# Kernel optimization log

Measured on AMD Instinct MI355X. Metric: run time of the kernel, lower is better.

## Reference

```python
import jax, jax.numpy as jnp
import numpy as np

B, SQ, SKV, E, H = 4, 2048, 2048, 1024, 16
HD = E // H  # 64


def stablemax(x):
    # StableMax: s(x) = x+1 if x>=0 else 1/(1-x), normalized along last axis
    s = jnp.where(x >= 0, x + 1.0, 1.0 / (1.0 - x))
    return s / jnp.sum(s, axis=-1, keepdims=True)


def setup_inputs() -> dict:
    key = jax.random.key(0)
    ks = jax.random.split(key, 6)
    scale = 1.0 / np.sqrt(E)
    return {
        "query": jax.random.normal(ks[0], (B, SQ, E), jnp.float32),
        "key_value": jax.random.normal(ks[1], (B, SKV, E), jnp.float32),
        "Wq": jax.random.normal(ks[2], (E, E), jnp.float32) * scale,
        "bq": jnp.zeros((E,), jnp.float32),
        "Wk": jax.random.normal(ks[3], (E, E), jnp.float32) * scale,
        "bk": jnp.zeros((E,), jnp.float32),
        "Wv": jax.random.normal(ks[4], (E, E), jnp.float32) * scale,
        "bv": jnp.zeros((E,), jnp.float32),
        "Wo": jax.random.normal(ks[5], (E, E), jnp.float32) * scale,
        "bo": jnp.zeros((E,), jnp.float32),
    }


def reference(query, key_value, Wq, bq, Wk, bk, Wv, bv, Wo, bo):
    b = query.shape[0]
    # linear projections (torch Linear: x @ W^T + b)
    q = query @ Wq.T + bq
    k = key_value @ Wk.T + bk
    v = key_value @ Wv.T + bv
    # [B, H, S, HD]
    q = q.reshape(b, -1, H, HD).transpose(0, 2, 1, 3)
    k = k.reshape(b, -1, H, HD).transpose(0, 2, 1, 3)
    v = v.reshape(b, -1, H, HD).transpose(0, 2, 1, 3)
    scores = jnp.einsum("bhqd,bhkd->bhqk", q, k) / np.sqrt(HD).astype(np.float32)
    attn = stablemax(scores)  # dropout is identity in eval mode
    context = jnp.einsum("bhqk,bhkd->bhqd", attn, v)
    context = context.transpose(0, 2, 1, 3).reshape(b, -1, E)
    return context @ Wo.T + bo
```

## Files before the change

kernel.cpp:

```cpp
#include <hip/hip_runtime.h>

typedef __bf16 bf16;
typedef __bf16 bf16x8 __attribute__((ext_vector_type(8)));
typedef __bf16 bf16x4 __attribute__((ext_vector_type(4)));
typedef __bf16 bf16x2 __attribute__((ext_vector_type(2)));
typedef float f32x4 __attribute__((ext_vector_type(4)));

__device__ __forceinline__ f32x4 mfma16(bf16x8 a, bf16x8 b, f32x4 c) {
    return __builtin_amdgcn_mfma_f32_16x16x32_bf16(a, b, c, 0, 0, 0);
}

#define GLOAD_LDS16(gp, lp)                                                    \
    __builtin_amdgcn_global_load_lds(                                          \
        (const __attribute__((address_space(1))) unsigned int*)(gp),           \
        (__attribute__((address_space(3))) unsigned int*)(lp), 16, 0, 0)

__global__ __launch_bounds__(256) void cast_inputs(
    const float* __restrict__ w0, const float* __restrict__ w1,
    const float* __restrict__ w2, const float* __restrict__ w3,
    const float* __restrict__ kv, bf16* __restrict__ Wb,
    bf16* __restrict__ KVa) {
    long i4 = (long)blockIdx.x * 256 + threadIdx.x;
    const float* src;
    bf16* dst;
    long loc;
    if (i4 < 1048576) {
        int which = (int)(i4 >> 18);
        loc = (i4 & 262143) << 2;
        src = which == 0 ? w0 : which == 1 ? w1 : which == 2 ? w2 : w3;
        dst = Wb + ((long)which << 20);
    } else {
        loc = (i4 - 1048576) << 2;
        src = kv;
        dst = KVa;
    }
    float4 f = *(const float4*)(src + loc);
    bf16x4 o;
    o[0] = (bf16)f.x; o[1] = (bf16)f.y; o[2] = (bf16)f.z; o[3] = (bf16)f.w;
    *(bf16x4*)(dst + loc) = o;
}

template <typename AT, int OM>
__global__ __launch_bounds__(256) void gemm_bt(
    const AT* __restrict__ A, const bf16* __restrict__ Wt,
    const float* __restrict__ bias, void* __restrict__ Yv) {
    constexpr int Kd = 1024, Nd = 1024;
    constexpr int TP = 132;
    __shared__ bf16 smem[OM == 2 ? 128 * TP : 8192];
    bf16* As = smem;
    bf16* Bs = smem + 4096;
    const int tid = threadIdx.x;
    const int wid = tid >> 6, lane = tid & 63;
    const int l16 = lane & 15, quad = lane >> 4;
    const int n0 = blockIdx.x * 128, m0 = blockIdx.y * 128;
    const int mh = (wid >> 1) * 64, nh = (wid & 1) * 64;

    f32x4 acc[4][4];
#pragma unroll
    for (int i = 0; i < 4; ++i)
#pragma unroll
        for (int j = 0; j < 4; ++j) acc[i][j] = (f32x4){0.f, 0.f, 0.f, 0.f};

    const int c0 = tid, c1 = tid + 256;
    const int sr = tid >> 1, sc = (tid & 1) * 16;

    for (int k0 = 0; k0 < Kd; k0 += 32) {
        GLOAD_LDS16(Wt + (long)(n0 + (c0 >> 2)) * Kd + k0 + (c0 & 3) * 8, &Bs[c0 * 8]);
        GLOAD_LDS16(Wt + (long)(n0 + (c1 >> 2)) * Kd + k0 + (c1 & 3) * 8, &Bs[(long)c1 * 8]);
        if constexpr (sizeof(AT) == 4) {
            const float* ap = (const float*)A + (long)(m0 + sr) * Kd + k0 + sc;
            float4 f0 = *(const float4*)(ap + 0);
            float4 f1 = *(const float4*)(ap + 4);
            float4 f2 = *(const float4*)(ap + 8);
            float4 f3 = *(const float4*)(ap + 12);
            bf16x8 p0, p1;
            p0[0] = (bf16)f0.x; p0[1] = (bf16)f0.y; p0[2] = (bf16)f0.z; p0[3] = (bf16)f0.w;
            p0[4] = (bf16)f1.x; p0[5] = (bf16)f1.y; p0[6] = (bf16)f1.z; p0[7] = (bf16)f1.w;
            p1[0] = (bf16)f2.x; p1[1] = (bf16)f2.y; p1[2] = (bf16)f2.z; p1[3] = (bf16)f2.w;
            p1[4] = (bf16)f3.x; p1[5] = (bf16)f3.y; p1[6] = (bf16)f3.z; p1[7] = (bf16)f3.w;
            *(bf16x8*)&As[sr * 32 + sc] = p0;
            *(bf16x8*)&As[sr * 32 + sc + 8] = p1;
        } else {
            GLOAD_LDS16((const bf16*)A + (long)(m0 + (c0 >> 2)) * Kd + k0 + (c0 & 3) * 8, &As[c0 * 8]);
            GLOAD_LDS16((const bf16*)A + (long)(m0 + (c1 >> 2)) * Kd + k0 + (c1 & 3) * 8, &As[(long)c1 * 8]);
        }
        __syncthreads();
        bf16x8 af[4], bq[4];
#pragma unroll
        for (int i = 0; i < 4; ++i)
            af[i] = *(const bf16x8*)&As[(mh + i * 16 + l16) * 32 + quad * 8];
#pragma unroll
        for (int i = 0; i < 4; ++i)
            bq[i] = *(const bf16x8*)&Bs[(nh + i * 16 + l16) * 32 + quad * 8];
#pragma unroll
        for (int i = 0; i < 4; ++i)
#pragma unroll
            for (int j = 0; j < 4; ++j)
                acc[i][j] = mfma16(af[i], bq[j], acc[i][j]);
        __syncthreads();
    }

    if constexpr (OM == 2) {
#pragma unroll
        for (int j = 0; j < 4; ++j) {
            const int col = nh + j * 16 + l16;
            const float bv = bias[n0 + col];
#pragma unroll
            for (int i = 0; i < 4; ++i)
#pragma unroll
                for (int p = 0; p < 2; ++p) {
                    bf16x2 pk2;
                    pk2[0] = (bf16)(acc[i][j][p * 2 + 0] + bv);
                    pk2[1] = (bf16)(acc[i][j][p * 2 + 1] + bv);
                    *(bf16x2*)&smem[col * TP + mh + i * 16 + quad * 4 + p * 2] = pk2;
                }
        }
        __syncthreads();
        const int b_ = m0 >> 11, skv0 = m0 & 2047;
        const int rowc = tid & 15;
#pragma unroll
        for (int c = 0; c < 8; ++c) {
            const int col = (tid >> 4) + c * 16;
            const int colg = n0 + col;
            bf16x8 v = *(const bf16x8*)&smem[col * TP + rowc * 8];
            const long base = ((long)((b_ * 16 + (colg >> 6)) * 64 + (colg & 63))) << 11;
            *(bf16x8*)((bf16*)Yv + base + skv0 + rowc * 8) = v;
        }
    } else {
#pragma unroll
        for (int j = 0; j < 4; ++j) {
            const int col = n0 + nh + j * 16 + l16;
            const float bv = bias[col];
#pragma unroll
            for (int i = 0; i < 4; ++i)
#pragma unroll
                for (int r = 0; r < 4; ++r) {
                    int row = m0 + mh + i * 16 + quad * 4 + r;
                    float v = acc[i][j][r] + bv;
                    if constexpr (OM == 1)
                        ((float*)Yv)[(long)row * Nd + col] = v;
                    else
                        ((bf16*)Yv)[(long)row * Nd + col] = (bf16)v;
                }
        }
    }
}

__global__ __launch_bounds__(256) void attn_kernel(
    const bf16* __restrict__ Q, const bf16* __restrict__ K,
    const bf16* __restrict__ Vt, bf16* __restrict__ C) {
    constexpr int E = 1024, S = 2048;
    __shared__ bf16 Ks[64 * 72];
    __shared__ bf16 VTs[64 * 72];
    __shared__ bf16 Ps[4][32 * 72];

    const int tid = threadIdx.x;
    const int wid = tid >> 6, lane = tid & 63;
    const int l16 = lane & 15, quad = lane >> 4;
    const int qt = blockIdx.x, h = blockIdx.y, b = blockIdx.z;

    const long q0 = (long)b * S + qt * 128;
    const bf16* Qg = Q + q0 * E + h * 64;
    const bf16* Kg = K + (long)b * S * E + h * 64;
    const bf16* Vg = Vt + ((long)(b * 16 + h) << 17);

    bf16x8 qf[2][2];
#pragma unroll
    for (int mt = 0; mt < 2; ++mt)
#pragma unroll
        for (int kc = 0; kc < 2; ++kc)
            qf[mt][kc] = *(const bf16x8*)(Qg + (long)(wid * 32 + mt * 16 + l16) * E + kc * 32 + quad * 8);

    f32x4 ctx[2][4];
    f32x4 den[2];
#pragma unroll
    for (int mt = 0; mt < 2; ++mt) {
        den[mt] = (f32x4){0.f, 0.f, 0.f, 0.f};
#pragma unroll
        for (int nt = 0; nt < 4; ++nt) ctx[mt][nt] = (f32x4){0.f, 0.f, 0.f, 0.f};
    }

    const int krow = tid >> 2, kcol = (tid & 3) * 16;

    for (int kv0 = 0; kv0 < S; kv0 += 64) {
        {
            const bf16* kp = Kg + (long)(kv0 + krow) * E + kcol;
            *(bf16x8*)&Ks[krow * 72 + kcol] = *(const bf16x8*)kp;
            *(bf16x8*)&Ks[krow * 72 + kcol + 8] = *(const bf16x8*)(kp + 8);
        }
        {
            const bf16* vp = Vg + (long)krow * S + kv0 + kcol;
            *(bf16x8*)&VTs[krow * 72 + kcol] = *(const bf16x8*)vp;
            *(bf16x8*)&VTs[krow * 72 + kcol + 8] = *(const bf16x8*)(vp + 8);
        }
        __syncthreads();

        bf16x8 kf[4][2];
#pragma unroll
        for (int nt = 0; nt < 4; ++nt)
#pragma unroll
            for (int kc = 0; kc < 2; ++kc)
                kf[nt][kc] = *(const bf16x8*)&Ks[(nt * 16 + l16) * 72 + kc * 32 + quad * 8];
        f32x4 sacc[2][4];
#pragma unroll
        for (int mt = 0; mt < 2; ++mt)
#pragma unroll
            for (int nt = 0; nt < 4; ++nt) sacc[mt][nt] = (f32x4){0.f, 0.f, 0.f, 0.f};
#pragma unroll
        for (int mt = 0; mt < 2; ++mt)
#pragma unroll
            for (int nt = 0; nt < 4; ++nt)
#pragma unroll
                for (int kc = 0; kc < 2; ++kc)
                    sacc[mt][nt] = mfma16(qf[mt][kc], kf[nt][kc], sacc[mt][nt]);

#pragma unroll
        for (int mt = 0; mt < 2; ++mt) {
#pragma unroll
            for (int nt = 0; nt < 4; ++nt) {
                f32x4 s;
#pragma unroll
                for (int r = 0; r < 4; ++r) {
                    float x = sacc[mt][nt][r];
                    float u = __builtin_fmaf(__builtin_fabsf(x), 0.125f, 1.0f);
                    float sv = (x >= 0.f) ? u : __builtin_amdgcn_rcpf(u);
                    s[r] = sv;
                    Ps[wid][(mt * 16 + quad * 4 + r) * 72 + nt * 16 + l16] = (bf16)sv;
                }
                den[mt] += s;
            }
        }

        bf16x8 pf[2][2], vf[4][2];
#pragma unroll
        for (int mt = 0; mt < 2; ++mt)
#pragma unroll
            for (int kc = 0; kc < 2; ++kc)
                pf[mt][kc] = *(const bf16x8*)&Ps[wid][(mt * 16 + l16) * 72 + kc * 32 + quad * 8];
#pragma unroll
        for (int nt = 0; nt < 4; ++nt)
#pragma unroll
            for (int kc = 0; kc < 2; ++kc)
                vf[nt][kc] = *(const bf16x8*)&VTs[(nt * 16 + l16) * 72 + kc * 32 + quad * 8];
#pragma unroll
        for (int mt = 0; mt < 2; ++mt)
#pragma unroll
            for (int nt = 0; nt < 4; ++nt)
#pragma unroll
                for (int kc = 0; kc < 2; ++kc)
                    ctx[mt][nt] = mfma16(pf[mt][kc], vf[nt][kc], ctx[mt][nt]);
        __syncthreads();
    }

#pragma unroll
    for (int mt = 0; mt < 2; ++mt) {
#pragma unroll
        for (int r = 0; r < 4; ++r) {
            float d = den[mt][r];
            d += __shfl_xor(d, 1, 16);
            d += __shfl_xor(d, 2, 16);
            d += __shfl_xor(d, 4, 16);
            d += __shfl_xor(d, 8, 16);
            den[mt][r] = d;
        }
    }

#pragma unroll
    for (int mt = 0; mt < 2; ++mt) {
#pragma unroll
        for (int nt = 0; nt < 4; ++nt) {
#pragma unroll
            for (int r = 0; r < 4; ++r) {
                int row = wid * 32 + mt * 16 + quad * 4 + r;
                float v = ctx[mt][nt][r] * __builtin_amdgcn_rcpf(den[mt][r]);
                C[(q0 + row) * E + h * 64 + nt * 16 + l16] = (bf16)v;
            }
        }
    }
}

extern "C" void kernel_launch(void* const* d_in, const int* in_sizes, int n_in,
                              void* d_out, int out_size, void* d_ws, size_t ws_size,
                              hipStream_t stream) {
    const float* query = (const float*)d_in[0];
    const float* keyv  = (const float*)d_in[1];
    const float* Wq = (const float*)d_in[2];
    const float* bq = (const float*)d_in[3];
    const float* Wk = (const float*)d_in[4];
    const float* bk = (const float*)d_in[5];
    const float* Wv = (const float*)d_in[6];
    const float* bv = (const float*)d_in[7];
    const float* Wo = (const float*)d_in[8];
    const float* bo = (const float*)d_in[9];

    char* ws = (char*)d_ws;
    bf16* Wb  = (bf16*)ws;
    bf16* KVa = (bf16*)(ws + (8l << 20));
    bf16* Qw  = (bf16*)(ws + (24l << 20));
    bf16* Kw  = (bf16*)(ws + (40l << 20));
    bf16* Vt  = (bf16*)(ws + (56l << 20));
    bf16* Cw  = KVa;

    cast_inputs<<<12288, 256, 0, stream>>>(Wq, Wk, Wv, Wo, keyv, Wb, KVa);

    dim3 gg(8, 64);
    gemm_bt<float, 0><<<gg, 256, 0, stream>>>(query, Wb, bq, Qw);
    gemm_bt<bf16, 0><<<gg, 256, 0, stream>>>(KVa, Wb + (1l << 20), bk, Kw);
    gemm_bt<bf16, 2><<<gg, 256, 0, stream>>>(KVa, Wb + (2l << 20), bv, Vt);

    attn_kernel<<<dim3(16, 16, 4), 256, 0, stream>>>(Qw, Kw, Vt, Cw);

    gemm_bt<bf16, 1><<<gg, 256, 0, stream>>>(Cw, Wb + (3l << 20), bo, (float*)d_out);
}
```

Before: 381.8 us.

## Keep attention probabilities in registers via transposed S and fp16 PV MFMA

Attention now computes S^T (K as the A operand), so the MFMA output layout feeds straight into the B operand of a 16x16x16 fp16 MFMA for P·V. This removes the per-wave LDS round trip for the probability tile. V is stored as fp16 so the PV MFMA can use it, and the KV tile grows to 128 rows per iteration, which halves the number of barriers. The denominator now reduces with cross-quad shuffles, and the output is staged through LDS so global writes are coalesced. In exchange, the PV MFMA has half the K depth per instruction, and fp16 gives P and V less range than bf16.

```diff
diff --git a/kernel.cpp b/kernel.cpp
--- a/kernel.cpp
+++ b/kernel.cpp
@@ -3,11 +3,17 @@
 typedef __bf16 bf16;
 typedef __bf16 bf16x8 __attribute__((ext_vector_type(8)));
 typedef __bf16 bf16x4 __attribute__((ext_vector_type(4)));
-typedef __bf16 bf16x2 __attribute__((ext_vector_type(2)));
+typedef _Float16 f16;
+typedef _Float16 f16x2 __attribute__((ext_vector_type(2)));
+typedef _Float16 f16x4 __attribute__((ext_vector_type(4)));
+typedef _Float16 f16x8 __attribute__((ext_vector_type(8)));
 typedef float f32x4 __attribute__((ext_vector_type(4)));
 
-__device__ __forceinline__ f32x4 mfma16(bf16x8 a, bf16x8 b, f32x4 c) {
+__device__ __forceinline__ f32x4 mfma_qk(bf16x8 a, bf16x8 b, f32x4 c) {
     return __builtin_amdgcn_mfma_f32_16x16x32_bf16(a, b, c, 0, 0, 0);
+}
+__device__ __forceinline__ f32x4 mfma_pv(f16x4 a, f16x4 b, f32x4 c) {
+    return __builtin_amdgcn_mfma_f32_16x16x16f16(a, b, c, 0, 0, 0);
 }
 
 #define GLOAD_LDS16(gp, lp)                                                    \
@@ -46,7 +52,7 @@
     const float* __restrict__ bias, void* __restrict__ Yv) {
     constexpr int Kd = 1024, Nd = 1024;
     constexpr int TP = 132;
-    __shared__ bf16 smem[OM == 2 ? 128 * TP : 8192];
+    __shared__ __align__(16) bf16 smem[OM == 2 ? 128 * TP : 8192];
     bf16* As = smem;
     bf16* Bs = smem + 4096;
     const int tid = threadIdx.x;
@@ -96,7 +102,7 @@
         for (int i = 0; i < 4; ++i)
 #pragma unroll
             for (int j = 0; j < 4; ++j)
-                acc[i][j] = mfma16(af[i], bq[j], acc[i][j]);
+                acc[i][j] = mfma_qk(af[i], bq[j], acc[i][j]);
         __syncthreads();
     }
 
@@ -109,10 +115,10 @@
             for (int i = 0; i < 4; ++i)
 #pragma unroll
                 for (int p = 0; p < 2; ++p) {
-                    bf16x2 pk2;
-                    pk2[0] = (bf16)(acc[i][j][p * 2 + 0] + bv);
-                    pk2[1] = (bf16)(acc[i][j][p * 2 + 1] + bv);
-                    *(bf16x2*)&smem[col * TP + mh + i * 16 + quad * 4 + p * 2] = pk2;
+                    f16x2 pk2;
+                    pk2[0] = (f16)(acc[i][j][p * 2 + 0] + bv);
+                    pk2[1] = (f16)(acc[i][j][p * 2 + 1] + bv);
+                    *(f16x2*)&smem[col * TP + mh + i * 16 + quad * 4 + p * 2] = pk2;
                 }
         }
         __syncthreads();
@@ -148,11 +154,10 @@
 
 __global__ __launch_bounds__(256) void attn_kernel(
     const bf16* __restrict__ Q, const bf16* __restrict__ K,
-    const bf16* __restrict__ Vt, bf16* __restrict__ C) {
+    const f16* __restrict__ Vt, bf16* __restrict__ C) {
     constexpr int E = 1024, S = 2048;
-    __shared__ bf16 Ks[64 * 72];
-    __shared__ bf16 VTs[64 * 72];
-    __shared__ bf16 Ps[4][32 * 72];
+    __shared__ __align__(16) bf16 Ks[128 * 72];
+    __shared__ __align__(16) f16 VTs[64 * 136];
 
     const int tid = threadIdx.x;
     const int wid = tid >> 6, lane = tid & 63;
@@ -162,7 +167,7 @@
     const long q0 = (long)b * S + qt * 128;
     const bf16* Qg = Q + q0 * E + h * 64;
     const bf16* Kg = K + (long)b * S * E + h * 64;
-    const bf16* Vg = Vt + ((long)(b * 16 + h) << 17);
+    const f16* Vg = Vt + ((long)(b * 16 + h) << 17);
 
     bf16x8 qf[2][2];
 #pragma unroll
@@ -172,110 +177,87 @@
             qf[mt][kc] = *(const bf16x8*)(Qg + (long)(wid * 32 + mt * 16 + l16) * E + kc * 32 + quad * 8);
 
     f32x4 ctx[2][4];
-    f32x4 den[2];
-#pragma unroll
-    for (int mt = 0; mt < 2; ++mt) {
-        den[mt] = (f32x4){0.f, 0.f, 0.f, 0.f};
-#pragma unroll
-        for (int nt = 0; nt < 4; ++nt) ctx[mt][nt] = (f32x4){0.f, 0.f, 0.f, 0.f};
-    }
-
-    const int krow = tid >> 2, kcol = (tid & 3) * 16;
-
-    for (int kv0 = 0; kv0 < S; kv0 += 64) {
+    float den[2] = {0.f, 0.f};
+#pragma unroll
+    for (int mt = 0; mt < 2; ++mt)
+#pragma unroll
+        for (int dt = 0; dt < 4; ++dt) ctx[mt][dt] = (f32x4){0.f, 0.f, 0.f, 0.f};
+
+    const int srow = tid >> 2, sq = tid & 3;
+
+    for (int kv0 = 0; kv0 < S; kv0 += 128) {
+#pragma unroll
+        for (int rr = 0; rr < 2; ++rr) {
+            const int r = rr * 64 + srow;
+            const bf16* kp = Kg + (long)(kv0 + r) * E + sq * 16;
+            *(bf16x8*)&Ks[r * 72 + sq * 16] = *(const bf16x8*)kp;
+            *(bf16x8*)&Ks[r * 72 + sq * 16 + 8] = *(const bf16x8*)(kp + 8);
+        }
         {
-            const bf16* kp = Kg + (long)(kv0 + krow) * E + kcol;
-            *(bf16x8*)&Ks[krow * 72 + kcol] = *(const bf16x8*)kp;
-            *(bf16x8*)&Ks[krow * 72 + kcol + 8] = *(const bf16x8*)(kp + 8);
-        }
-        {
-            const bf16* vp = Vg + (long)krow * S + kv0 + kcol;
-            *(bf16x8*)&VTs[krow * 72 + kcol] = *(const bf16x8*)vp;
-            *(bf16x8*)&VTs[krow * 72 + kcol + 8] = *(const bf16x8*)(vp + 8);
-        }
-        __syncthreads();
-
-        bf16x8 kf[4][2];
-#pragma unroll
-        for (int nt = 0; nt < 4; ++nt)
-#pragma unroll
-            for (int kc = 0; kc < 2; ++kc)
-                kf[nt][kc] = *(const bf16x8*)&Ks[(nt * 16 + l16) * 72 + kc * 32 + quad * 8];
-        f32x4 sacc[2][4];
-#pragma unroll
-        for (int mt = 0; mt < 2; ++mt)
-#pragma unroll
-            for (int nt = 0; nt < 4; ++nt) sacc[mt][nt] = (f32x4){0.f, 0.f, 0.f, 0.f};
-#pragma unroll
-        for (int mt = 0; mt < 2; ++mt)
-#pragma unroll
-            for (int nt = 0; nt < 4; ++nt)
-#pragma unroll
-                for (int kc = 0; kc < 2; ++kc)
-                    sacc[mt][nt] = mfma16(qf[mt][kc], kf[nt][kc], sacc[mt][nt]);
-
-#pragma unroll
-        for (int mt = 0; mt < 2; ++mt) {
-#pragma unroll
-            for (int nt = 0; nt < 4; ++nt) {
-                f32x4 s;
+            const f16* vp = Vg + (long)srow * S + kv0 + sq * 32;
+            *(f16x8*)&VTs[srow * 136 + sq * 32 + 0]  = *(const f16x8*)(vp + 0);
+            *(f16x8*)&VTs[srow * 136 + sq * 32 + 8]  = *(const f16x8*)(vp + 8);
+            *(f16x8*)&VTs[srow * 136 + sq * 32 + 16] = *(const f16x8*)(vp + 16);
+            *(f16x8*)&VTs[srow * 136 + sq * 32 + 24] = *(const f16x8*)(vp + 24);
+        }
+        __syncthreads();
+
+#pragma unroll
+        for (int kvm = 0; kvm < 8; ++kvm) {
+            bf16x8 kf0 = *(const bf16x8*)&Ks[(kvm * 16 + l16) * 72 + quad * 8];
+            bf16x8 kf1 = *(const bf16x8*)&Ks[(kvm * 16 + l16) * 72 + 32 + quad * 8];
+
+            f16x4 pp[2];
+#pragma unroll
+            for (int mt = 0; mt < 2; ++mt) {
+                f32x4 sacc = mfma_qk(kf0, qf[mt][0], (f32x4){0.f, 0.f, 0.f, 0.f});
+                sacc = mfma_qk(kf1, qf[mt][1], sacc);
 #pragma unroll
                 for (int r = 0; r < 4; ++r) {
-                    float x = sacc[mt][nt][r];
+                    float x = sacc[r];
                     float u = __builtin_fmaf(__builtin_fabsf(x), 0.125f, 1.0f);
                     float sv = (x >= 0.f) ? u : __builtin_amdgcn_rcpf(u);
-                    s[r] = sv;
-                    Ps[wid][(mt * 16 + quad * 4 + r) * 72 + nt * 16 + l16] = (bf16)sv;
+                    den[mt] += sv;
+                    pp[mt][r] = (f16)sv;
                 }
-                den[mt] += s;
             }
-        }
-
-        bf16x8 pf[2][2], vf[4][2];
-#pragma unroll
-        for (int mt = 0; mt < 2; ++mt)
-#pragma unroll
-            for (int kc = 0; kc < 2; ++kc)
-                pf[mt][kc] = *(const bf16x8*)&Ps[wid][(mt * 16 + l16) * 72 + kc * 32 + quad * 8];
-#pragma unroll
-        for (int nt = 0; nt < 4; ++nt)
-#pragma unroll
-            for (int kc = 0; kc < 2; ++kc)
-                vf[nt][kc] = *(const bf16x8*)&VTs[(nt * 16 + l16) * 72 + kc * 32 + quad * 8];
-#pragma unroll
-        for (int mt = 0; mt < 2; ++mt)
-#pragma unroll
-            for (int nt = 0; nt < 4; ++nt)
-#pragma unroll
-                for (int kc = 0; kc < 2; ++kc)
-                    ctx[mt][nt] = mfma16(pf[mt][kc], vf[nt][kc], ctx[mt][nt]);
-        __syncthreads();
-    }
-
+#pragma unroll
+            for (int dt = 0; dt < 4; ++dt) {
+                f16x4 vf = *(const f16x4*)&VTs[(dt * 16 + l16) * 136 + kvm * 16 + quad * 4];
+#pragma unroll
+                for (int mt = 0; mt < 2; ++mt)
+                    ctx[mt][dt] = mfma_pv(vf, pp[mt], ctx[mt][dt]);
+            }
+        }
+        __syncthreads();
+    }
+
+    float scl[2];
 #pragma unroll
     for (int mt = 0; mt < 2; ++mt) {
-#pragma unroll
-        for (int r = 0; r < 4; ++r) {
-            float d = den[mt][r];
-            d += __shfl_xor(d, 1, 16);
-            d += __shfl_xor(d, 2, 16);
-            d += __shfl_xor(d, 4, 16);
-            d += __shfl_xor(d, 8, 16);
-            den[mt][r] = d;
-        }
-    }
-
-#pragma unroll
-    for (int mt = 0; mt < 2; ++mt) {
-#pragma unroll
-        for (int nt = 0; nt < 4; ++nt) {
-#pragma unroll
-            for (int r = 0; r < 4; ++r) {
-                int row = wid * 32 + mt * 16 + quad * 4 + r;
-                float v = ctx[mt][nt][r] * __builtin_amdgcn_rcpf(den[mt][r]);
-                C[(q0 + row) * E + h * 64 + nt * 16 + l16] = (bf16)v;
-            }
-        }
+        float d = den[mt];
+        d += __shfl_xor(d, 16);
+        d += __shfl_xor(d, 32);
+        scl[mt] = __builtin_amdgcn_rcpf(d);
+    }
+
+    bf16* Os = Ks;
+#pragma unroll
+    for (int mt = 0; mt < 2; ++mt)
+#pragma unroll
+        for (int dt = 0; dt < 4; ++dt) {
+            bf16x4 o;
+#pragma unroll
+            for (int r = 0; r < 4; ++r) o[r] = (bf16)(ctx[mt][dt][r] * scl[mt]);
+            *(bf16x4*)&Os[(wid * 32 + mt * 16 + l16) * 68 + dt * 16 + quad * 4] = o;
+        }
+    __syncthreads();
+    {
+        const int r = tid >> 1, c = (tid & 1) * 32;
+        bf16* cp = C + (q0 + r) * E + h * 64 + c;
+#pragma unroll
+        for (int j = 0; j < 4; ++j)
+            *(bf16x8*)(cp + j * 8) = *(const bf16x8*)&Os[r * 68 + c + j * 8];
     }
 }
 
@@ -298,7 +280,7 @@
     bf16* KVa = (bf16*)(ws + (8l << 20));
     bf16* Qw  = (bf16*)(ws + (24l << 20));
     bf16* Kw  = (bf16*)(ws + (40l << 20));
-    bf16* Vt  = (bf16*)(ws + (56l << 20));
+    f16*  Vt  = (f16*)(ws + (56l << 20));
     bf16* Cw  = KVa;
 
     cast_inputs<<<12288, 256, 0, stream>>>(Wq, Wk, Wv, Wo, keyv, Wb, KVa);
```

Result: slower. 392.2 us (+2.7%).
